# Optimization experiments

Measured on AMD Instinct MI355X. Metric: run time of the kernel, lower is better.

The kernel has to match this reference:

```python
import jax, jax.numpy as jnp
import numpy as np

N, E, G, R = 65536, 524288, 1024, 512
D_IN, H, R_FEAT, NH, HD = 7, 128, 25, 4, 32
EPS = 1e-5


def setup_inputs() -> dict:
    key = jax.random.key(0)
    ks = jax.random.split(key, 16)
    f = lambda i, shape, s: jax.random.normal(ks[i], shape, jnp.float32) * s
    return {
        "x": jax.random.normal(ks[0], (N, D_IN), jnp.float32),
        "edge_index": jax.random.randint(ks[1], (2, E), 0, N),
        "batch": jnp.repeat(jnp.arange(G), N // G),  # 64 atoms per graph, sorted
        "per_residue_features": jax.random.normal(ks[2], (R, R_FEAT), jnp.float32),
        # GCN layer weights (PyG GCNConv: x @ W then normalized aggregation, + bias)
        "W0": f(3, (D_IN, H), 0.3), "b0": jnp.zeros(H, jnp.float32),
        "W1": f(4, (H, H), 0.1), "b1": jnp.zeros(H, jnp.float32),
        "W2": f(5, (H, H), 0.1), "b2": jnp.zeros(H, jnp.float32),
        # BatchNorm (eval mode, running stats)
        "bn_gamma": jnp.ones((3, H), jnp.float32),
        "bn_beta": jnp.zeros((3, H), jnp.float32),
        "bn_mean": f(6, (3, H), 0.1),
        "bn_var": jax.random.uniform(ks[7], (3, H), jnp.float32) + 0.5,
        # residue projection
        "res_W": f(8, (R_FEAT, H), 0.2), "res_b": jnp.zeros(H, jnp.float32),
        # MultiheadAttention packed in-proj (rows: q, k, v) and out-proj
        "in_W": f(9, (3 * H, H), 0.08), "in_b": jnp.zeros(3 * H, jnp.float32),
        "out_W": f(10, (H, H), 0.08), "out_b": jnp.zeros(H, jnp.float32),
        # classifier 128 -> 64 -> 1
        "cls_W1": f(11, (H, 64), 0.1), "cls_b1": jnp.zeros(64, jnp.float32),
        "cls_W2": f(12, (64, 1), 0.1), "cls_b2": jnp.zeros(1, jnp.float32),
    }


def reference(x, edge_index, batch, per_residue_features,
              W0, b0, W1, b1, W2, b2,
              bn_gamma, bn_beta, bn_mean, bn_var,
              res_W, res_b, in_W, in_b, out_W, out_b,
              cls_W1, cls_b1, cls_W2, cls_b2):
    src, dst = edge_index[0], edge_index[1]
    # GCN symmetric norm with self-loops: deg[i] = 1 + in-degree(i)
    deg = jnp.ones(N, x.dtype).at[dst].add(1.0)
    dinv = jax.lax.rsqrt(deg)
    enorm = (dinv[src] * dinv[dst])[:, None]      # [E,1]
    self_norm = (dinv * dinv)[:, None]            # [N,1]

    def gcn_bn_relu(h, W, b, i):
        m = h @ W                                  # [N,H]
        agg = m * self_norm
        agg = agg.at[dst].add(m[src] * enorm) + b
        y = bn_gamma[i] * (agg - bn_mean[i]) * jax.lax.rsqrt(bn_var[i] + EPS) + bn_beta[i]
        return jax.nn.relu(y)  # dropout is identity at inference

    h = gcn_bn_relu(x, W0, b0, 0)
    h = gcn_bn_relu(h, W1, b1, 1)
    h = gcn_bn_relu(h, W2, b2, 2)

    # shared residue KV (same for every graph) -> fused attention over all nodes
    res = per_residue_features @ res_W + res_b     # [R,H]
    Wq, Wk, Wv = jnp.split(in_W, 3, axis=0)
    bq, bk, bv = jnp.split(in_b, 3)
    q = (h @ Wq.T + bq).reshape(N, NH, HD)
    k = (res @ Wk.T + bk).reshape(R, NH, HD)
    v = (res @ Wv.T + bv).reshape(R, NH, HD)
    scores = jnp.einsum('nhd,rhd->nhr', q, k) / np.float32(np.sqrt(HD))
    attn = jax.nn.softmax(scores, axis=-1)         # [N,NH,R]
    o = jnp.einsum('nhr,rhd->nhd', attn, v).reshape(N, H)
    o = o @ out_W.T + out_b                        # [N,H]

    # per-graph mean pool (segment mean over batch ids)
    counts = jnp.zeros(G, o.dtype).at[batch].add(1.0)
    pooled = jnp.zeros((G, H), o.dtype).at[batch].add(o) / counts[:, None]

    hid = jax.nn.relu(pooled @ cls_W1 + cls_b1)
    logits = (hid @ cls_W2 + cls_b2)[:, 0]         # [G]
    return logits
```

## Files before the change

kernel.cpp:

```cpp
#include <hip/hip_runtime.h>
#include <math.h>

#define N_NODES 65536
#define N_EDGES 524288
#define N_GRAPHS 1024
#define H 128
#define R_RES 512
#define NH 4
#define HD 32
#define D_IN 7
#define EPS 1e-5f

typedef __attribute__((ext_vector_type(8))) short short8;
typedef __attribute__((ext_vector_type(4))) short short4v;
typedef __attribute__((ext_vector_type(4))) float f32x4;
typedef __attribute__((ext_vector_type(4))) unsigned uint4v;
typedef __attribute__((ext_vector_type(2))) unsigned uint2v;
typedef __attribute__((ext_vector_type(4))) unsigned short us4;

#if __has_builtin(__builtin_amdgcn_exp2f)
#define EXP2F __builtin_amdgcn_exp2f
#else
#define EXP2F exp2f
#endif
#if __has_builtin(__builtin_amdgcn_rcpf)
#define RCPF __builtin_amdgcn_rcpf
#else
#define RCPF(x) (1.0f/(x))
#endif

__device__ __forceinline__ f32x4 mfma_k16(short4v a, short4v b, f32x4 c){
#if defined(__HIP_DEVICE_COMPILE__)
  return __builtin_amdgcn_mfma_f32_16x16x16bf16_1k(a, b, c, 0, 0, 0);
#else
  (void)a; (void)b; return c;
#endif
}

__device__ __forceinline__ unsigned short rnd_bf16(float f){
  return (unsigned short)((__builtin_bit_cast(unsigned, f) + 0x8000u) >> 16);
}
__device__ __forceinline__ unsigned pk_bf16(float lo, float hi){
  unsigned a = __builtin_bit_cast(unsigned, lo) + 0x8000u;
  unsigned b = __builtin_bit_cast(unsigned, hi) + 0x8000u;
  return __builtin_amdgcn_perm(b, a, 0x07060302u);
}
__device__ __forceinline__ float bflo(unsigned u){ return __builtin_bit_cast(float, u << 16); }
__device__ __forceinline__ float bfhi(unsigned u){ return __builtin_bit_cast(float, u & 0xFFFF0000u); }

__global__ __launch_bounds__(256) void k_count(const int* __restrict__ dst, int* __restrict__ cnt, int E){
  int e = blockIdx.x*256 + threadIdx.x;
  if (e < E) atomicAdd(&cnt[dst[e]], 1);
}

__global__ __launch_bounds__(256) void k_part(const int* __restrict__ cnt, int* __restrict__ part){
  int i = blockIdx.x*256 + threadIdx.x;
  int v = cnt[i];
  #pragma unroll
  for (int off=1; off<64; off<<=1) v += __shfl_xor(v, off);
  __shared__ int red[4];
  if ((threadIdx.x & 63) == 0) red[threadIdx.x >> 6] = v;
  __syncthreads();
  if (threadIdx.x == 0) part[blockIdx.x] = red[0]+red[1]+red[2]+red[3];
}

__global__ __launch_bounds__(256) void k_scanp(int* __restrict__ part){
  __shared__ int s[256];
  int t = threadIdx.x;
  int v = part[t];
  s[t] = v;
  __syncthreads();
  for (int off=1; off<256; off<<=1){
    int u = (t >= off) ? s[t-off] : 0;
    __syncthreads();
    s[t] += u;
    __syncthreads();
  }
  part[t] = s[t] - v;
}

__global__ __launch_bounds__(256) void k_apply(const int* __restrict__ cnt, const int* __restrict__ part,
      int* __restrict__ csr_off, int* __restrict__ cursor, float* __restrict__ dinv){
  __shared__ int s[256];
  int b = blockIdx.x, t = threadIdx.x;
  int i = b*256 + t;
  int c = cnt[i];
  s[t] = c;
  __syncthreads();
  for (int off=1; off<256; off<<=1){
    int u = (t >= off) ? s[t-off] : 0;
    __syncthreads();
    s[t] += u;
    __syncthreads();
  }
  int o0 = part[b] + s[t] - c;
  csr_off[i] = o0;
  cursor[i] = o0;
  dinv[i] = rsqrtf(1.0f + (float)c);
  if (i == N_NODES-1) csr_off[N_NODES] = N_EDGES;
}

__global__ __launch_bounds__(256) void k_fill(const int* __restrict__ src, const int* __restrict__ dst,
      const float* __restrict__ dinv, int* __restrict__ cursor,
      int* __restrict__ csr_src, float* __restrict__ csr_w, int E){
  int e = blockIdx.x*256 + threadIdx.x;
  if (e >= E) return;
  int s = src[e], d = dst[e];
  int p = atomicAdd(&cursor[d], 1);
  csr_src[p] = s;
  csr_w[p] = dinv[s]*dinv[d];
}

__global__ __launch_bounds__(256) void k_lin0(const float* __restrict__ x, const float* __restrict__ W0,
                                              unsigned short* __restrict__ out){
  int gid = blockIdx.x*256 + threadIdx.x;
  int l = threadIdx.x & 63;
  int n = __builtin_amdgcn_readfirstlane(gid >> 6);
  float a0 = 0.0f, a1 = 0.0f;
  #pragma unroll
  for (int k=0;k<D_IN;k++){
    float xv = x[(long)n*D_IN + k];
    float2 wv = *(const float2*)(W0 + k*H + 2*l);
    a0 = fmaf(xv, wv.x, a0); a1 = fmaf(xv, wv.y, a1);
  }
  *(unsigned*)(out + (long)n*H + 2*l) = pk_bf16(a0, a1);
}

__global__ __launch_bounds__(256) void k_gemm_mfma(const unsigned short* __restrict__ A,
      const float* __restrict__ Bsrc, const float* __restrict__ bias, void* __restrict__ Cout,
      int transB, int outMode){
  __shared__ unsigned short Bt[128][136];
  int tid = threadIdx.x;
  long rowBase = (long)blockIdx.x * 128;
  int w = tid >> 6, l = tid & 63;
  int lc = l & 15, q4 = l >> 4;

  if (transB){
    for (int i = tid; i < 4096; i += 256){
      int c = i >> 5, seg = i & 31;
      float4 v = *(const float4*)(Bsrc + (long)c*128 + seg*4);
      uint2 p; p.x = pk_bf16(v.x, v.y); p.y = pk_bf16(v.z, v.w);
      *(uint2*)&Bt[c][seg*4] = p;
    }
  } else {
    for (int i = tid; i < 4096; i += 256){
      int k = i >> 5, seg = i & 31;
      float4 v = *(const float4*)(Bsrc + (long)k*128 + seg*4);
      Bt[seg*4+0][k] = rnd_bf16(v.x); Bt[seg*4+1][k] = rnd_bf16(v.y);
      Bt[seg*4+2][k] = rnd_bf16(v.z); Bt[seg*4+3][k] = rnd_bf16(v.w);
    }
  }

  short8 af[2][4];
  #pragma unroll
  for (int rt=0;rt<2;rt++){
    long row = rowBase + w*32 + rt*16 + lc;
    #pragma unroll
    for (int kc=0;kc<4;kc++)
      af[rt][kc] = *(const short8*)(A + row*128 + kc*32 + q4*8);
  }

  f32x4 acc[2][8];
  #pragma unroll
  for (int rt=0;rt<2;rt++)
    #pragma unroll
    for (int ct=0;ct<8;ct++) acc[rt][ct] = (f32x4){0.f,0.f,0.f,0.f};

  __syncthreads();

  #pragma unroll
  for (int kc=0;kc<4;kc++){
    #pragma unroll
    for (int ct=0;ct<8;ct++){
      short8 bf = *(const short8*)&Bt[ct*16 + lc][kc*32 + q4*8];
      acc[0][ct] = __builtin_amdgcn_mfma_f32_16x16x32_bf16(af[0][kc], bf, acc[0][ct], 0,0,0);
      acc[1][ct] = __builtin_amdgcn_mfma_f32_16x16x32_bf16(af[1][kc], bf, acc[1][ct], 0,0,0);
    }
  }

  float bv[8];
  #pragma unroll
  for (int ct=0;ct<8;ct++) bv[ct] = bias ? bias[ct*16 + lc] : 0.0f;
  #pragma unroll
  for (int rt=0;rt<2;rt++){
    #pragma unroll
    for (int ct=0;ct<8;ct++){
      int col = ct*16 + lc;
      float vv[4];
      #pragma unroll
      for (int i=0;i<4;i++) vv[i] = acc[rt][ct][i] + bv[ct];
      long row0 = rowBase + w*32 + rt*16 + q4*4;
      if (outMode == 0){
        #pragma unroll
        for (int i=0;i<4;i++) ((unsigned short*)Cout)[(row0+i)*128 + col] = rnd_bf16(vv[i]);
      } else if (outMode == 1){
        #pragma unroll
        for (int i=0;i<4;i++) ((float*)Cout)[(row0+i)*128 + col] = vv[i];
      } else {
        us4 p = {rnd_bf16(vv[0]), rnd_bf16(vv[1]), rnd_bf16(vv[2]), rnd_bf16(vv[3])};
        *(us4*)((unsigned short*)Cout + (long)col*512 + row0) = p;
      }
    }
  }
}

__global__ __launch_bounds__(256) void k_rpk(const unsigned short* __restrict__ K,
                                             unsigned short* __restrict__ F){
  int t = blockIdx.x*256 + threadIdx.x;
  int r = t >> 7, d = t & 127;
  int h = d >> 5, q4d = (d >> 3) & 3, j = d & 7;
  int rc = r >> 4, lc = r & 15;
  F[(((long)(h*32 + rc)*64) + q4d*16 + lc)*8 + j] = K[t];
}
__global__ __launch_bounds__(256) void k_rpv(const unsigned short* __restrict__ Vt,
                                             unsigned short* __restrict__ F){
  int t = blockIdx.x*256 + threadIdx.x;
  int j = t & 3, half = (t >> 2) & 1, lc = (t >> 3) & 15, q4 = (t >> 7) & 3, rc = (t >> 9) & 31, h = t >> 14;
  F[t] = Vt[(long)(h*32 + half*16 + lc)*512 + rc*16 + q4*4 + j];
}

__global__ __launch_bounds__(256) void k_agg(const unsigned short* __restrict__ m, const int* __restrict__ csr_off,
      const int* __restrict__ csr_src, const float* __restrict__ csr_w, const float* __restrict__ dinv,
      const float* __restrict__ b, const float* __restrict__ gamma, const float* __restrict__ beta,
      const float* __restrict__ mean, const float* __restrict__ var, unsigned short* __restrict__ out){
  int gt = blockIdx.x*256 + threadIdx.x;
  int li = gt & 15;
  int n = gt >> 4;
  int c = li*8;
  float dn = dinv[n], sn = dn*dn;
  float a[8];
  {
    uint4v u = *(const uint4v*)(m + (long)n*H + c);
    a[0]=bflo(u.x)*sn; a[1]=bfhi(u.x)*sn; a[2]=bflo(u.y)*sn; a[3]=bfhi(u.y)*sn;
    a[4]=bflo(u.z)*sn; a[5]=bfhi(u.z)*sn; a[6]=bflo(u.w)*sn; a[7]=bfhi(u.w)*sn;
  }
  int e0 = csr_off[n], e1 = csr_off[n+1];
  int e = e0;
  for (; e + 2 <= e1; e += 2){
    int s0 = csr_src[e],  s1 = csr_src[e+1];
    float w0 = csr_w[e],  w1 = csr_w[e+1];
    uint4v u0 = *(const uint4v*)(m + (long)s0*H + c);
    uint4v u1 = *(const uint4v*)(m + (long)s1*H + c);
    a[0]=fmaf(bflo(u0.x),w0,a[0]); a[1]=fmaf(bfhi(u0.x),w0,a[1]);
    a[2]=fmaf(bflo(u0.y),w0,a[2]); a[3]=fmaf(bfhi(u0.y),w0,a[3]);
    a[4]=fmaf(bflo(u0.z),w0,a[4]); a[5]=fmaf(bfhi(u0.z),w0,a[5]);
    a[6]=fmaf(bflo(u0.w),w0,a[6]); a[7]=fmaf(bfhi(u0.w),w0,a[7]);
    a[0]=fmaf(bflo(u1.x),w1,a[0]); a[1]=fmaf(bfhi(u1.x),w1,a[1]);
    a[2]=fmaf(bflo(u1.y),w1,a[2]); a[3]=fmaf(bfhi(u1.y),w1,a[3]);
    a[4]=fmaf(bflo(u1.z),w1,a[4]); a[5]=fmaf(bfhi(u1.z),w1,a[5]);
    a[6]=fmaf(bflo(u1.w),w1,a[6]); a[7]=fmaf(bfhi(u1.w),w1,a[7]);
  }
  if (e < e1){
    int s0 = csr_src[e]; float w0 = csr_w[e];
    uint4v u0 = *(const uint4v*)(m + (long)s0*H + c);
    a[0]=fmaf(bflo(u0.x),w0,a[0]); a[1]=fmaf(bfhi(u0.x),w0,a[1]);
    a[2]=fmaf(bflo(u0.y),w0,a[2]); a[3]=fmaf(bfhi(u0.y),w0,a[3]);
    a[4]=fmaf(bflo(u0.z),w0,a[4]); a[5]=fmaf(bfhi(u0.z),w0,a[5]);
    a[6]=fmaf(bflo(u0.w),w0,a[6]); a[7]=fmaf(bfhi(u0.w),w0,a[7]);
  }
  float4 g0 = *(const float4*)(gamma + c), g1 = *(const float4*)(gamma + c + 4);
  float4 v0 = *(const float4*)(var   + c), v1 = *(const float4*)(var   + c + 4);
  float4 b0 = *(const float4*)(b     + c), b1 = *(const float4*)(b     + c + 4);
  float4 m0 = *(const float4*)(mean  + c), m1 = *(const float4*)(mean  + c + 4);
  float4 t0 = *(const float4*)(beta  + c), t1 = *(const float4*)(beta  + c + 4);
  float r[8];
  r[0]=fmaxf(g0.x*rsqrtf(v0.x+EPS)*(a[0]+b0.x-m0.x)+t0.x, 0.f);
  r[1]=fmaxf(g0.y*rsqrtf(v0.y+EPS)*(a[1]+b0.y-m0.y)+t0.y, 0.f);
  r[2]=fmaxf(g0.z*rsqrtf(v0.z+EPS)*(a[2]+b0.z-m0.z)+t0.z, 0.f);
  r[3]=fmaxf(g0.w*rsqrtf(v0.w+EPS)*(a[3]+b0.w-m0.w)+t0.w, 0.f);
  r[4]=fmaxf(g1.x*rsqrtf(v1.x+EPS)*(a[4]+b1.x-m1.x)+t1.x, 0.f);
  r[5]=fmaxf(g1.y*rsqrtf(v1.y+EPS)*(a[5]+b1.y-m1.y)+t1.y, 0.f);
  r[6]=fmaxf(g1.z*rsqrtf(v1.z+EPS)*(a[6]+b1.z-m1.z)+t1.z, 0.f);
  r[7]=fmaxf(g1.w*rsqrtf(v1.w+EPS)*(a[7]+b1.w-m1.w)+t1.w, 0.f);
  uint4v p;
  p.x = pk_bf16(r[0],r[1]); p.y = pk_bf16(r[2],r[3]);
  p.z = pk_bf16(r[4],r[5]); p.w = pk_bf16(r[6],r[7]);
  *(uint4v*)(out + (long)n*H + c) = p;
}

__global__ __launch_bounds__(256,2) void k_gemm(const float* __restrict__ A, const float* __restrict__ B,
      const float* __restrict__ bias, void* __restrict__ C, int K, int transB, int outBf16){
  __shared__ float Bs[128][132];
  __shared__ float As[16][128];
  int tid = threadIdx.x;
  long rowBase = (long)blockIdx.x * 128;

  if (!transB){
    for (int idx = tid; idx < 128*128; idx += 256){
      int k = idx >> 7, c = idx & 127;
      Bs[k][c] = (k < K) ? B[(long)k*128 + c] : 0.0f;
    }
  } else {
    for (int idx = tid; idx < 128*128; idx += 256){
      int c = idx >> 7, k = idx & 127;
      Bs[k][c] = (k < K) ? B[(long)c*K + k] : 0.0f;
    }
  }

  float acc[8][8];
  #pragma unroll
  for (int i=0;i<8;i++)
    #pragma unroll
    for (int j=0;j<8;j++) acc[i][j] = 0.0f;

  int rg = tid >> 4, cg = tid & 15;
  int r0 = rg*8, c0 = cg*8;
  int srow = tid >> 1, skoff = (tid & 1)*8;
  const bool fast = ((K & 15) == 0);

  for (int k0 = 0; k0 < K; k0 += 16){
    __syncthreads();
    const float* ap = A + (rowBase + srow)*K + k0 + skoff;
    if (fast){
      float4 v0 = *(const float4*)(ap);
      float4 v1 = *(const float4*)(ap + 4);
      As[skoff+0][srow] = v0.x; As[skoff+1][srow] = v0.y;
      As[skoff+2][srow] = v0.z; As[skoff+3][srow] = v0.w;
      As[skoff+4][srow] = v1.x; As[skoff+5][srow] = v1.y;
      As[skoff+6][srow] = v1.z; As[skoff+7][srow] = v1.w;
    } else {
      #pragma unroll
      for (int j=0;j<8;j++){
        int kk = k0 + skoff + j;
        As[skoff+j][srow] = (kk < K) ? ap[j] : 0.0f;
      }
    }
    __syncthreads();
    #pragma unroll
    for (int k=0;k<16;k++){
      float4 a0 = *(const float4*)(&As[k][r0]);
      float4 a1 = *(const float4*)(&As[k][r0+4]);
      float4 b0 = *(const float4*)(&Bs[k0+k][c0]);
      float4 b1 = *(const float4*)(&Bs[k0+k][c0+4]);
      float a[8] = {a0.x,a0.y,a0.z,a0.w,a1.x,a1.y,a1.z,a1.w};
      float b[8] = {b0.x,b0.y,b0.z,b0.w,b1.x,b1.y,b1.z,b1.w};
      #pragma unroll
      for (int i=0;i<8;i++)
        #pragma unroll
        for (int j=0;j<8;j++)
          acc[i][j] = fmaf(a[i], b[j], acc[i][j]);
    }
  }

  #pragma unroll
  for (int i=0;i<8;i++){
    float o[8];
    #pragma unroll
    for (int j=0;j<8;j++) o[j] = acc[i][j] + (bias ? bias[c0+j] : 0.0f);
    long row = rowBase + r0 + i;
    if (outBf16){
      uint4v p;
      p.x = pk_bf16(o[0],o[1]); p.y = pk_bf16(o[2],o[3]);
      p.z = pk_bf16(o[4],o[5]); p.w = pk_bf16(o[6],o[7]);
      *(uint4v*)((unsigned short*)C + row*128 + c0) = p;
    } else {
      float* cp = (float*)C + row*128 + c0;
      *(float4*)cp = (float4){o[0],o[1],o[2],o[3]};
      *(float4*)(cp+4) = (float4){o[4],o[5],o[6],o[7]};
    }
  }
}

__global__ __launch_bounds__(256,8) void k_attn(const unsigned short* __restrict__ hb,
      const float* __restrict__ inW, const float* __restrict__ inb,
      const unsigned short* __restrict__ Kf, const unsigned short* __restrict__ Vf,
      unsigned short* __restrict__ obuf){
  int tid = threadIdx.x;
  int h = blockIdx.y;
  int w = tid >> 6, l = tid & 63;
  int lc = l & 15, q4 = l >> 4;
  long nb = (long)blockIdx.x*128 + w*32;
  const float scale = 0.25503489f;

  int srcA = lc + (q4 & 1)*32;
  int srcB = srcA + 16;
  bool hi = (q4 >> 1) != 0;

  short8 wq[2][4];
  #pragma unroll
  for (int t=0;t<2;t++){
    #pragma unroll
    for (int kc=0;kc<4;kc++){
      const float* wp = inW + (long)(h*32 + t*16 + lc)*128 + kc*32 + q4*8;
      float4 x0 = *(const float4*)wp;
      float4 x1 = *(const float4*)(wp+4);
      uint4v p; p.x = pk_bf16(x0.x,x0.y); p.y = pk_bf16(x0.z,x0.w);
      p.z = pk_bf16(x1.x,x1.y); p.w = pk_bf16(x1.z,x1.w);
      wq[t][kc] = __builtin_bit_cast(short8, p);
    }
  }
  float bq0[4], bq1[4];
  #pragma unroll
  for (int i=0;i<4;i++){ bq0[i] = inb[h*32 + q4*4 + i]; bq1[i] = inb[h*32 + 16 + q4*4 + i]; }

  short8 qB[2];
  #pragma unroll
  for (int nt=0;nt<2;nt++){
    short8 hf[4];
    #pragma unroll
    for (int kc=0;kc<4;kc++)
      hf[kc] = *(const short8*)(hb + (nb + nt*16 + lc)*128 + kc*32 + q4*8);
    f32x4 qa0 = (f32x4){0.f,0.f,0.f,0.f};
    f32x4 qa1 = (f32x4){0.f,0.f,0.f,0.f};
    #pragma unroll
    for (int kc=0;kc<4;kc++){
      qa0 = __builtin_amdgcn_mfma_f32_16x16x32_bf16(wq[0][kc], hf[kc], qa0, 0,0,0);
      qa1 = __builtin_amdgcn_mfma_f32_16x16x32_bf16(wq[1][kc], hf[kc], qa1, 0,0,0);
    }
    unsigned P0 = pk_bf16((qa0[0]+bq0[0])*scale, (qa0[1]+bq0[1])*scale);
    unsigned P1 = pk_bf16((qa0[2]+bq0[2])*scale, (qa0[3]+bq0[3])*scale);
    unsigned P2 = pk_bf16((qa1[0]+bq1[0])*scale, (qa1[1]+bq1[1])*scale);
    unsigned P3 = pk_bf16((qa1[2]+bq1[2])*scale, (qa1[3]+bq1[3])*scale);
    unsigned x0 = __shfl(P0, srcA), x1 = __shfl(P1, srcA), x2 = __shfl(P2, srcA), x3 = __shfl(P3, srcA);
    unsigned y0 = __shfl(P0, srcB), y1 = __shfl(P1, srcB), y2 = __shfl(P2, srcB), y3 = __shfl(P3, srcB);
    uint4v bp; bp.x = hi?x2:x0; bp.y = hi?x3:x1; bp.z = hi?y2:y0; bp.w = hi?y3:y1;
    qB[nt] = __builtin_bit_cast(short8, bp);
  }

  const short4v ones4 = {(short)0x3F80,(short)0x3F80,(short)0x3F80,(short)0x3F80};
  f32x4 oA[2], oB[2], os[2];
  #pragma unroll
  for (int nt=0;nt<2;nt++){
    oA[nt] = (f32x4){0.f,0.f,0.f,0.f};
    oB[nt] = (f32x4){0.f,0.f,0.f,0.f};
    os[nt] = (f32x4){0.f,0.f,0.f,0.f};
  }

  const unsigned short* Kp = Kf + (long)h*16384 + (long)l*8;
  const unsigned short* Vp = Vf + (long)h*16384 + (long)l*8;

  for (int rc = 0; rc < 32; rc++){
    short8 kf = *(const short8*)(Kp + rc*512);
    uint4v vv = *(const uint4v*)(Vp + rc*512);
    uint2v va = {vv.x, vv.y}, vb = {vv.z, vv.w};
    short4v vfA = __builtin_bit_cast(short4v, va);
    short4v vfB = __builtin_bit_cast(short4v, vb);
    #pragma unroll
    for (int nt=0;nt<2;nt++){
      f32x4 z = {0.f,0.f,0.f,0.f};
      f32x4 s = __builtin_amdgcn_mfma_f32_16x16x32_bf16(kf, qB[nt], z, 0,0,0);
      float e0 = EXP2F(s[0]), e1 = EXP2F(s[1]), e2 = EXP2F(s[2]), e3 = EXP2F(s[3]);
      uint2v pk2; pk2.x = pk_bf16(e0, e1); pk2.y = pk_bf16(e2, e3);
      short4v pf = __builtin_bit_cast(short4v, pk2);
      oA[nt] = mfma_k16(vfA,   pf, oA[nt]);
      oB[nt] = mfma_k16(vfB,   pf, oB[nt]);
      os[nt] = mfma_k16(ones4, pf, os[nt]);
    }
  }

  #pragma unroll
  for (int nt=0;nt<2;nt++){
    float inv = RCPF(os[nt][0]);
    long node = nb + nt*16 + lc;
    us4 a = { rnd_bf16(oA[nt][0]*inv), rnd_bf16(oA[nt][1]*inv),
              rnd_bf16(oA[nt][2]*inv), rnd_bf16(oA[nt][3]*inv) };
    us4 b = { rnd_bf16(oB[nt][0]*inv), rnd_bf16(oB[nt][1]*inv),
              rnd_bf16(oB[nt][2]*inv), rnd_bf16(oB[nt][3]*inv) };
    *(us4*)(obuf + node*128 + h*32 + q4*4) = a;
    *(us4*)(obuf + node*128 + h*32 + 16 + q4*4) = b;
  }
}

__global__ __launch_bounds__(256) void k_gemm_out(const unsigned short* __restrict__ A,
      const float* __restrict__ Bsrc, const float* __restrict__ bias,
      const float* __restrict__ W1, const float* __restrict__ b1,
      const float* __restrict__ W2, const float* __restrict__ b2, float* __restrict__ out){
  __shared__ unsigned short Bt[128][136];
  __shared__ float pools[4][128];
  __shared__ float pooled[2][128];
  int tid = threadIdx.x;
  long rowBase = (long)blockIdx.x * 128;
  int w = tid >> 6, l = tid & 63;
  int lc = l & 15, q4 = l >> 4;

  for (int i = tid; i < 4096; i += 256){
    int c = i >> 5, seg = i & 31;
    float4 v = *(const float4*)(Bsrc + (long)c*128 + seg*4);
    uint2 p; p.x = pk_bf16(v.x, v.y); p.y = pk_bf16(v.z, v.w);
    *(uint2*)&Bt[c][seg*4] = p;
  }

  short8 af[2][4];
  #pragma unroll
  for (int rt=0;rt<2;rt++){
    long row = rowBase + w*32 + rt*16 + lc;
    #pragma unroll
    for (int kc=0;kc<4;kc++)
      af[rt][kc] = *(const short8*)(A + row*128 + kc*32 + q4*8);
  }

  f32x4 acc[2][8];
  #pragma unroll
  for (int rt=0;rt<2;rt++)
    #pragma unroll
    for (int ct=0;ct<8;ct++) acc[rt][ct] = (f32x4){0.f,0.f,0.f,0.f};

  __syncthreads();

  #pragma unroll
  for (int kc=0;kc<4;kc++){
    #pragma unroll
    for (int ct=0;ct<8;ct++){
      short8 bf = *(const short8*)&Bt[ct*16 + lc][kc*32 + q4*8];
      acc[0][ct] = __builtin_amdgcn_mfma_f32_16x16x32_bf16(af[0][kc], bf, acc[0][ct], 0,0,0);
      acc[1][ct] = __builtin_amdgcn_mfma_f32_16x16x32_bf16(af[1][kc], bf, acc[1][ct], 0,0,0);
    }
  }

  #pragma unroll
  for (int ct=0;ct<8;ct++){
    float ps = acc[0][ct][0]+acc[0][ct][1]+acc[0][ct][2]+acc[0][ct][3]
             + acc[1][ct][0]+acc[1][ct][1]+acc[1][ct][2]+acc[1][ct][3];
    ps += __shfl_xor(ps, 16);
    ps += __shfl_xor(ps, 32);
    if (q4 == 0) pools[w][ct*16 + lc] = ps;
  }
  __syncthreads();

  if (tid < 128){
    int c = tid;
    pooled[0][c] = (pools[0][c] + pools[1][c]) * (1.0f/64.0f) + bias[c];
    pooled[1][c] = (pools[2][c] + pools[3][c]) * (1.0f/64.0f) + bias[c];
  }
  __syncthreads();

  if (tid < 128){
    int g = tid >> 6, tp = tid & 63;
    float hh = b1[tp];
    for (int c=0;c<128;c++) hh = fmaf(pooled[g][c], W1[c*64 + tp], hh);
    hh = fmaxf(hh, 0.0f);
    float v = hh * W2[tp];
    #pragma unroll
    for (int off=32; off>0; off>>=1) v += __shfl_down(v, off);
    if (tp == 0) out[blockIdx.x*2 + g] = v + b2[0];
  }
}

extern "C" void kernel_launch(void* const* d_in, const int* in_sizes, int n_in,
                              void* d_out, int out_size, void* d_ws, size_t ws_size,
                              hipStream_t stream){
  const float* x     = (const float*)d_in[0];
  const int*   ei    = (const int*)d_in[1];
  const float* perres= (const float*)d_in[3];
  const float* W0 = (const float*)d_in[4];
  const float* b0 = (const float*)d_in[5];
  const float* W1 = (const float*)d_in[6];  const float* b1 = (const float*)d_in[7];
  const float* W2 = (const float*)d_in[8];  const float* b2 = (const float*)d_in[9];
  const float* bng = (const float*)d_in[10]; const float* bnb = (const float*)d_in[11];
  const float* bnm = (const float*)d_in[12]; const float* bnv = (const float*)d_in[13];
  const float* resW = (const float*)d_in[14]; const float* resb = (const float*)d_in[15];
  const float* inW  = (const float*)d_in[16]; const float* inb  = (const float*)d_in[17];
  const float* outW = (const float*)d_in[18]; const float* outb = (const float*)d_in[19];
  const float* cW1 = (const float*)d_in[20]; const float* cb1 = (const float*)d_in[21];
  const float* cW2 = (const float*)d_in[22]; const float* cb2 = (const float*)d_in[23];
  float* out = (float*)d_out;

  char* ws = (char*)d_ws;
  size_t off = 0;
  auto alloc = [&](size_t bytes) -> char* {
    char* p = ws + off;
    off += (bytes + 255) & ~(size_t)255;
    return p;
  };
  float* dinv    = (float*)alloc((size_t)N_NODES*4);
  int*   cnt     = (int*)  alloc((size_t)N_NODES*4);
  int*   cursor  = (int*)  alloc((size_t)N_NODES*4);
  int*   csr_off = (int*)  alloc((size_t)(N_NODES+1)*4);
  int*   csr_src = (int*)  alloc((size_t)N_EDGES*4);
  float* csr_w   = (float*)alloc((size_t)N_EDGES*4);
  int*   part    = (int*)  alloc((size_t)256*4);
  unsigned short* mb  = (unsigned short*)alloc((size_t)N_NODES*H*2);
  unsigned short* hb  = (unsigned short*)alloc((size_t)N_NODES*H*2);
  unsigned short* resbuf = (unsigned short*)alloc((size_t)R_RES*H*2);
  unsigned short* Kbf = (unsigned short*)alloc((size_t)R_RES*H*2);
  unsigned short* Vtb = (unsigned short*)alloc((size_t)H*R_RES*2);
  unsigned short* Kfr = (unsigned short*)alloc((size_t)R_RES*H*2);
  unsigned short* Vfr = (unsigned short*)alloc((size_t)H*R_RES*2);
  if (off > ws_size) return;

  const int* srcI = ei;
  const int* dstI = ei + N_EDGES;

  (void)hipMemsetAsync(cnt, 0, (size_t)N_NODES*4, stream);
  k_count<<<N_EDGES/256, 256, 0, stream>>>(dstI, cnt, N_EDGES);
  k_part <<<N_NODES/256, 256, 0, stream>>>(cnt, part);
  k_scanp<<<1, 256, 0, stream>>>(part);
  k_apply<<<N_NODES/256, 256, 0, stream>>>(cnt, part, csr_off, cursor, dinv);
  k_fill <<<N_EDGES/256, 256, 0, stream>>>(srcI, dstI, dinv, cursor, csr_src, csr_w, N_EDGES);

  const int NB = N_NODES/128;
  const int AGB = N_NODES/16;
  k_lin0<<<N_NODES/4, 256, 0, stream>>>(x, W0, mb);
  k_agg<<<AGB, 256, 0, stream>>>(mb, csr_off, csr_src, csr_w, dinv, b0, bng,     bnb,     bnm,     bnv,     hb);
  k_gemm_mfma<<<NB, 256, 0, stream>>>(hb, W1, nullptr, mb, 0, 0);
  k_agg<<<AGB, 256, 0, stream>>>(mb, csr_off, csr_src, csr_w, dinv, b1, bng+128, bnb+128, bnm+128, bnv+128, hb);
  k_gemm_mfma<<<NB, 256, 0, stream>>>(hb, W2, nullptr, mb, 0, 0);
  k_agg<<<AGB, 256, 0, stream>>>(mb, csr_off, csr_src, csr_w, dinv, b2, bng+256, bnb+256, bnm+256, bnv+256, hb);

  k_gemm<<<R_RES/128, 256, 0, stream>>>(perres, resW, resb, resbuf, 25, 0, 1);
  k_gemm_mfma<<<R_RES/128, 256, 0, stream>>>(resbuf, inW + 128*128, inb + 128, Kbf, 1, 0);
  k_gemm_mfma<<<R_RES/128, 256, 0, stream>>>(resbuf, inW + 256*128, inb + 256, Vtb, 1, 2);
  k_rpk<<<(R_RES*H)/256, 256, 0, stream>>>(Kbf, Kfr);
  k_rpv<<<(R_RES*H)/256, 256, 0, stream>>>(Vtb, Vfr);

  dim3 agrid(N_NODES/128, NH);
  k_attn<<<agrid, 256, 0, stream>>>(hb, inW, inb, Kfr, Vfr, mb);

  k_gemm_out<<<NB, 256, 0, stream>>>(mb, outW, outb, cW1, cb1, cW2, cb2, out);
}
```

Baseline: 404.5 us.

## Pack CSR edges, unroll aggregation by four, merge repack kernels, widen attention tiles

Stores each CSR edge's source index and weight together as one int2 record, so aggregation issues a single 8-byte load per edge instead of two separate loads. The aggregation loop is unrolled to four edges to keep more gathers in flight. The K and V fragment repack kernels are merged into one launch. The attention kernel now handles 64 nodes per wave instead of 32 to reuse the K/V fragments more, which raises register use and lowers the occupancy hint.

```diff
diff --git a/kernel.cpp b/kernel.cpp
--- a/kernel.cpp
+++ b/kernel.cpp
@@ -47,6 +47,13 @@
 }
 __device__ __forceinline__ float bflo(unsigned u){ return __builtin_bit_cast(float, u << 16); }
 __device__ __forceinline__ float bfhi(unsigned u){ return __builtin_bit_cast(float, u & 0xFFFF0000u); }
+
+__device__ __forceinline__ void acc8(float* a, uint4v u, float wgt){
+  a[0]=fmaf(bflo(u.x),wgt,a[0]); a[1]=fmaf(bfhi(u.x),wgt,a[1]);
+  a[2]=fmaf(bflo(u.y),wgt,a[2]); a[3]=fmaf(bfhi(u.y),wgt,a[3]);
+  a[4]=fmaf(bflo(u.z),wgt,a[4]); a[5]=fmaf(bfhi(u.z),wgt,a[5]);
+  a[6]=fmaf(bflo(u.w),wgt,a[6]); a[7]=fmaf(bfhi(u.w),wgt,a[7]);
+}
 
 __global__ __launch_bounds__(256) void k_count(const int* __restrict__ dst, int* __restrict__ cnt, int E){
   int e = blockIdx.x*256 + threadIdx.x;
@@ -101,14 +108,15 @@
 }
 
 __global__ __launch_bounds__(256) void k_fill(const int* __restrict__ src, const int* __restrict__ dst,
-      const float* __restrict__ dinv, int* __restrict__ cursor,
-      int* __restrict__ csr_src, float* __restrict__ csr_w, int E){
+      const float* __restrict__ dinv, int* __restrict__ cursor, int2* __restrict__ csr_ev, int E){
   int e = blockIdx.x*256 + threadIdx.x;
   if (e >= E) return;
   int s = src[e], d = dst[e];
   int p = atomicAdd(&cursor[d], 1);
-  csr_src[p] = s;
-  csr_w[p] = dinv[s]*dinv[d];
+  int2 rec;
+  rec.x = s;
+  rec.y = __builtin_bit_cast(int, dinv[s]*dinv[d]);
+  csr_ev[p] = rec;
 }
 
 __global__ __launch_bounds__(256) void k_lin0(const float* __restrict__ x, const float* __restrict__ W0,
@@ -204,23 +212,24 @@
   }
 }
 
-__global__ __launch_bounds__(256) void k_rpk(const unsigned short* __restrict__ K,
-                                             unsigned short* __restrict__ F){
-  int t = blockIdx.x*256 + threadIdx.x;
-  int r = t >> 7, d = t & 127;
-  int h = d >> 5, q4d = (d >> 3) & 3, j = d & 7;
-  int rc = r >> 4, lc = r & 15;
-  F[(((long)(h*32 + rc)*64) + q4d*16 + lc)*8 + j] = K[t];
-}
-__global__ __launch_bounds__(256) void k_rpv(const unsigned short* __restrict__ Vt,
-                                             unsigned short* __restrict__ F){
-  int t = blockIdx.x*256 + threadIdx.x;
-  int j = t & 3, half = (t >> 2) & 1, lc = (t >> 3) & 15, q4 = (t >> 7) & 3, rc = (t >> 9) & 31, h = t >> 14;
-  F[t] = Vt[(long)(h*32 + half*16 + lc)*512 + rc*16 + q4*4 + j];
+__global__ __launch_bounds__(256) void k_rp(const unsigned short* __restrict__ K,
+      const unsigned short* __restrict__ Vt, unsigned short* __restrict__ FK,
+      unsigned short* __restrict__ FV){
+  int blk = blockIdx.x;
+  int t = (blk & 255)*256 + threadIdx.x;
+  if (blk < 256){
+    int r = t >> 7, d = t & 127;
+    int h = d >> 5, q4d = (d >> 3) & 3, j = d & 7;
+    int rc = r >> 4, lc = r & 15;
+    FK[(((long)(h*32 + rc)*64) + q4d*16 + lc)*8 + j] = K[t];
+  } else {
+    int j = t & 3, half = (t >> 2) & 1, lc = (t >> 3) & 15, q4 = (t >> 7) & 3, rc = (t >> 9) & 31, h = t >> 14;
+    FV[t] = Vt[(long)(h*32 + half*16 + lc)*512 + rc*16 + q4*4 + j];
+  }
 }
 
 __global__ __launch_bounds__(256) void k_agg(const unsigned short* __restrict__ m, const int* __restrict__ csr_off,
-      const int* __restrict__ csr_src, const float* __restrict__ csr_w, const float* __restrict__ dinv,
+      const int2* __restrict__ csr_ev, const float* __restrict__ dinv,
       const float* __restrict__ b, const float* __restrict__ gamma, const float* __restrict__ beta,
       const float* __restrict__ mean, const float* __restrict__ var, unsigned short* __restrict__ out){
   int gt = blockIdx.x*256 + threadIdx.x;
@@ -236,27 +245,22 @@
   }
   int e0 = csr_off[n], e1 = csr_off[n+1];
   int e = e0;
-  for (; e + 2 <= e1; e += 2){
-    int s0 = csr_src[e],  s1 = csr_src[e+1];
-    float w0 = csr_w[e],  w1 = csr_w[e+1];
-    uint4v u0 = *(const uint4v*)(m + (long)s0*H + c);
-    uint4v u1 = *(const uint4v*)(m + (long)s1*H + c);
-    a[0]=fmaf(bflo(u0.x),w0,a[0]); a[1]=fmaf(bfhi(u0.x),w0,a[1]);
-    a[2]=fmaf(bflo(u0.y),w0,a[2]); a[3]=fmaf(bfhi(u0.y),w0,a[3]);
-    a[4]=fmaf(bflo(u0.z),w0,a[4]); a[5]=fmaf(bfhi(u0.z),w0,a[5]);
-    a[6]=fmaf(bflo(u0.w),w0,a[6]); a[7]=fmaf(bfhi(u0.w),w0,a[7]);
-    a[0]=fmaf(bflo(u1.x),w1,a[0]); a[1]=fmaf(bfhi(u1.x),w1,a[1]);
-    a[2]=fmaf(bflo(u1.y),w1,a[2]); a[3]=fmaf(bfhi(u1.y),w1,a[3]);
-    a[4]=fmaf(bflo(u1.z),w1,a[4]); a[5]=fmaf(bfhi(u1.z),w1,a[5]);
-    a[6]=fmaf(bflo(u1.w),w1,a[6]); a[7]=fmaf(bfhi(u1.w),w1,a[7]);
-  }
-  if (e < e1){
-    int s0 = csr_src[e]; float w0 = csr_w[e];
-    uint4v u0 = *(const uint4v*)(m + (long)s0*H + c);
-    a[0]=fmaf(bflo(u0.x),w0,a[0]); a[1]=fmaf(bfhi(u0.x),w0,a[1]);
-    a[2]=fmaf(bflo(u0.y),w0,a[2]); a[3]=fmaf(bfhi(u0.y),w0,a[3]);
-    a[4]=fmaf(bflo(u0.z),w0,a[4]); a[5]=fmaf(bfhi(u0.z),w0,a[5]);
-    a[6]=fmaf(bflo(u0.w),w0,a[6]); a[7]=fmaf(bfhi(u0.w),w0,a[7]);
+  for (; e + 4 <= e1; e += 4){
+    int2 p0 = csr_ev[e],   p1 = csr_ev[e+1];
+    int2 p2 = csr_ev[e+2], p3 = csr_ev[e+3];
+    uint4v u0 = *(const uint4v*)(m + (long)p0.x*H + c);
+    uint4v u1 = *(const uint4v*)(m + (long)p1.x*H + c);
+    uint4v u2 = *(const uint4v*)(m + (long)p2.x*H + c);
+    uint4v u3 = *(const uint4v*)(m + (long)p3.x*H + c);
+    acc8(a, u0, __builtin_bit_cast(float, p0.y));
+    acc8(a, u1, __builtin_bit_cast(float, p1.y));
+    acc8(a, u2, __builtin_bit_cast(float, p2.y));
+    acc8(a, u3, __builtin_bit_cast(float, p3.y));
+  }
+  for (; e < e1; e++){
+    int2 p0 = csr_ev[e];
+    uint4v u0 = *(const uint4v*)(m + (long)p0.x*H + c);
+    acc8(a, u0, __builtin_bit_cast(float, p0.y));
   }
   float4 g0 = *(const float4*)(gamma + c), g1 = *(const float4*)(gamma + c + 4);
   float4 v0 = *(const float4*)(var   + c), v1 = *(const float4*)(var   + c + 4);
@@ -361,7 +365,7 @@
   }
 }
 
-__global__ __launch_bounds__(256,8) void k_attn(const unsigned short* __restrict__ hb,
+__global__ __launch_bounds__(256,4) void k_attn(const unsigned short* __restrict__ hb,
       const float* __restrict__ inW, const float* __restrict__ inb,
       const unsigned short* __restrict__ Kf, const unsigned short* __restrict__ Vf,
       unsigned short* __restrict__ obuf){
@@ -369,7 +373,7 @@
   int h = blockIdx.y;
   int w = tid >> 6, l = tid & 63;
   int lc = l & 15, q4 = l >> 4;
-  long nb = (long)blockIdx.x*128 + w*32;
+  long nb = (long)blockIdx.x*256 + w*64;
   const float scale = 0.25503489f;
 
   int srcA = lc + (q4 & 1)*32;
@@ -393,9 +397,9 @@
   #pragma unroll
   for (int i=0;i<4;i++){ bq0[i] = inb[h*32 + q4*4 + i]; bq1[i] = inb[h*32 + 16 + q4*4 + i]; }
 
-  short8 qB[2];
-  #pragma unroll
-  for (int nt=0;nt<2;nt++){
+  short8 qB[4];
+  #pragma unroll
+  for (int nt=0;nt<4;nt++){
     short8 hf[4];
     #pragma unroll
     for (int kc=0;kc<4;kc++)
@@ -418,9 +422,9 @@
   }
 
   const short4v ones4 = {(short)0x3F80,(short)0x3F80,(short)0x3F80,(short)0x3F80};
-  f32x4 oA[2], oB[2], os[2];
-  #pragma unroll
-  for (int nt=0;nt<2;nt++){
+  f32x4 oA[4], oB[4], os[4];
+  #pragma unroll
+  for (int nt=0;nt<4;nt++){
     oA[nt] = (f32x4){0.f,0.f,0.f,0.f};
     oB[nt] = (f32x4){0.f,0.f,0.f,0.f};
     os[nt] = (f32x4){0.f,0.f,0.f,0.f};
@@ -436,7 +440,7 @@
     short4v vfA = __builtin_bit_cast(short4v, va);
     short4v vfB = __builtin_bit_cast(short4v, vb);
     #pragma unroll
-    for (int nt=0;nt<2;nt++){
+    for (int nt=0;nt<4;nt++){
       f32x4 z = {0.f,0.f,0.f,0.f};
       f32x4 s = __builtin_amdgcn_mfma_f32_16x16x32_bf16(kf, qB[nt], z, 0,0,0);
       float e0 = EXP2F(s[0]), e1 = EXP2F(s[1]), e2 = EXP2F(s[2]), e3 = EXP2F(s[3]);
@@ -449,7 +453,7 @@
   }
 
   #pragma unroll
-  for (int nt=0;nt<2;nt++){
+  for (int nt=0;nt<4;nt++){
     float inv = RCPF(os[nt][0]);
     long node = nb + nt*16 + lc;
     us4 a = { rnd_bf16(oA[nt][0]*inv), rnd_bf16(oA[nt][1]*inv),
@@ -566,8 +570,7 @@
   int*   cnt     = (int*)  alloc((size_t)N_NODES*4);
   int*   cursor  = (int*)  alloc((size_t)N_NODES*4);
   int*   csr_off = (int*)  alloc((size_t)(N_NODES+1)*4);
-  int*   csr_src = (int*)  alloc((size_t)N_EDGES*4);
-  float* csr_w   = (float*)alloc((size_t)N_EDGES*4);
+  int2*  csr_ev  = (int2*) alloc((size_t)N_EDGES*8);
   int*   part    = (int*)  alloc((size_t)256*4);
   unsigned short* mb  = (unsigned short*)alloc((size_t)N_NODES*H*2);
   unsigned short* hb  = (unsigned short*)alloc((size_t)N_NODES*H*2);
@@ -586,24 +589,23 @@
   k_part <<<N_NODES/256, 256, 0, stream>>>(cnt, part);
   k_scanp<<<1, 256, 0, stream>>>(part);
   k_apply<<<N_NODES/256, 256, 0, stream>>>(cnt, part, csr_off, cursor, dinv);
-  k_fill <<<N_EDGES/256, 256, 0, stream>>>(srcI, dstI, dinv, cursor, csr_src, csr_w, N_EDGES);
+  k_fill <<<N_EDGES/256, 256, 0, stream>>>(srcI, dstI, dinv, cursor, csr_ev, N_EDGES);
 
   const int NB = N_NODES/128;
   const int AGB = N_NODES/16;
   k_lin0<<<N_NODES/4, 256, 0, stream>>>(x, W0, mb);
-  k_agg<<<AGB, 256, 0, stream>>>(mb, csr_off, csr_src, csr_w, dinv, b0, bng,     bnb,     bnm,     bnv,     hb);
+  k_agg<<<AGB, 256, 0, stream>>>(mb, csr_off, csr_ev, dinv, b0, bng,     bnb,     bnm,     bnv,     hb);
   k_gemm_mfma<<<NB, 256, 0, stream>>>(hb, W1, nullptr, mb, 0, 0);
-  k_agg<<<AGB, 256, 0, stream>>>(mb, csr_off, csr_src, csr_w, dinv, b1, bng+128, bnb+128, bnm+128, bnv+128, hb);
+  k_agg<<<AGB, 256, 0, stream>>>(mb, csr_off, csr_ev, dinv, b1, bng+128, bnb+128, bnm+128, bnv+128, hb);
   k_gemm_mfma<<<NB, 256, 0, stream>>>(hb, W2, nullptr, mb, 0, 0);
-  k_agg<<<AGB, 256, 0, stream>>>(mb, csr_off, csr_src, csr_w, dinv, b2, bng+256, bnb+256, bnm+256, bnv+256, hb);
+  k_agg<<<AGB, 256, 0, stream>>>(mb, csr_off, csr_ev, dinv, b2, bng+256, bnb+256, bnm+256, bnv+256, hb);
 
   k_gemm<<<R_RES/128, 256, 0, stream>>>(perres, resW, resb, resbuf, 25, 0, 1);
   k_gemm_mfma<<<R_RES/128, 256, 0, stream>>>(resbuf, inW + 128*128, inb + 128, Kbf, 1, 0);
   k_gemm_mfma<<<R_RES/128, 256, 0, stream>>>(resbuf, inW + 256*128, inb + 256, Vtb, 1, 2);
-  k_rpk<<<(R_RES*H)/256, 256, 0, stream>>>(Kbf, Kfr);
-  k_rpv<<<(R_RES*H)/256, 256, 0, stream>>>(Vtb, Vfr);
-
-  dim3 agrid(N_NODES/128, NH);
+  k_rp<<<512, 256, 0, stream>>>(Kbf, Vtb, Kfr, Vfr);
+
+  dim3 agrid(N_NODES/256, NH);
   k_attn<<<agrid, 256, 0, stream>>>(hb, inW, inb, Kfr, Vfr, mb);
 
   k_gemm_out<<<NB, 256, 0, stream>>>(mb, outW, outb, cW1, cb1, cW2, cb2, out);
```

Result: faster. 388.6 us (-3.9%).
